# Optimization experiments

Measured on AMD Instinct MI355X. Metric: run time of the kernel, lower is better.

Reference implementation:

```python
import jax, jax.numpy as jnp
import numpy as np

INPUT_DIM = 24
HIDDEN = 128
NUM_LAYERS = 3
OUTPUT_DIM = 1


def _lstm_layer(x, Wih, Whh, bih, bhh):
    """Single LSTM layer, PyTorch gate order (i, f, g, o). x: [B,T,D] -> [B,T,H]."""
    B = x.shape[0]
    H = Whh.shape[1]
    # Precompute input projections for all timesteps at once: [B,T,4H]
    xg = jnp.einsum('btd,gd->btg', x, Wih) + bih
    xg = jnp.swapaxes(xg, 0, 1)  # [T,B,4H]
    h0 = jnp.zeros((B, H), x.dtype)
    c0 = jnp.zeros((B, H), x.dtype)

    def step(carry, xt):
        h, c = carry
        gates = xt + h @ Whh.T + bhh  # [B,4H]
        i, f, g, o = jnp.split(gates, 4, axis=-1)
        i = jax.nn.sigmoid(i)
        f = jax.nn.sigmoid(f)
        g = jnp.tanh(g)
        o = jax.nn.sigmoid(o)
        c = f * c + i * g
        h = o * jnp.tanh(c)
        return (h, c), h

    _, hs = jax.lax.scan(step, (h0, c0), xg)  # hs: [T,B,H]
    return jnp.swapaxes(hs, 0, 1)  # [B,T,H]


def setup_inputs() -> dict:
    key = jax.random.key(0)
    ks = jax.random.split(key, 16)
    B, T = 2048, 256
    s = 0.05
    inp = {
        'x': jax.random.normal(ks[0], (B, T, INPUT_DIM), dtype=jnp.float32),
    }
    dims_in = [INPUT_DIM, HIDDEN, HIDDEN]
    for l in range(NUM_LAYERS):
        inp[f'Wih{l}'] = jax.random.normal(ks[1 + 4 * l], (4 * HIDDEN, dims_in[l]), dtype=jnp.float32) * s
        inp[f'Whh{l}'] = jax.random.normal(ks[2 + 4 * l], (4 * HIDDEN, HIDDEN), dtype=jnp.float32) * s
        inp[f'bih{l}'] = jax.random.normal(ks[3 + 4 * l], (4 * HIDDEN,), dtype=jnp.float32) * s
        inp[f'bhh{l}'] = jax.random.normal(ks[4 + 4 * l], (4 * HIDDEN,), dtype=jnp.float32) * s
    inp['Wfc'] = jax.random.normal(ks[13], (OUTPUT_DIM, HIDDEN), dtype=jnp.float32) * s
    inp['bfc'] = jax.random.normal(ks[14], (OUTPUT_DIM,), dtype=jnp.float32) * s
    return inp


def reference(x, Wih0, Whh0, bih0, bhh0, Wih1, Whh1, bih1, bhh1,
              Wih2, Whh2, bih2, bhh2, Wfc, bfc):
    # 3 stacked LSTM layers (dropout inactive in eval mode), zero initial state.
    h = _lstm_layer(x, Wih0, Whh0, bih0, bhh0)
    h = _lstm_layer(h, Wih1, Whh1, bih1, bhh1)
    h = _lstm_layer(h, Wih2, Whh2, bih2, bhh2)
    # Linear projection of the final timestep: [B,1]
    return h[:, -1, :] @ Wfc.T + bfc
```

## Files before the change

### kernel.cpp

```cpp
#include <hip/hip_runtime.h>

#define T_STEPS 256
#define BATCH   2048
#define HID     128
#define ROWS    8

typedef short short8  __attribute__((ext_vector_type(8)));
typedef float float4v __attribute__((ext_vector_type(4)));

__device__ __forceinline__ unsigned short f2bf(float f) {
    unsigned int u = __builtin_bit_cast(unsigned int, f);
    u += 0x7fffu + ((u >> 16) & 1u);
    return (unsigned short)(u >> 16);
}
__device__ __forceinline__ float bf2f(unsigned short b) {
    unsigned int u = ((unsigned int)b) << 16;
    return __builtin_bit_cast(float, u);
}

#if __has_builtin(__builtin_amdgcn_exp2f)
#define EXP2F(x) __builtin_amdgcn_exp2f(x)
#else
#define EXP2F(x) exp2f(x)
#endif
__device__ __forceinline__ float sigf(float x) {
    return __builtin_amdgcn_rcpf(1.0f + EXP2F(x * -1.442695041f));
}
__device__ __forceinline__ float tanh_fast(float x) {
    return 2.0f * __builtin_amdgcn_rcpf(1.0f + EXP2F(x * -2.885390082f)) - 1.0f;
}

__device__ __forceinline__ void block_sync_lds() {
    asm volatile("s_waitcnt lgkmcnt(0)" ::: "memory");
    __builtin_amdgcn_s_barrier();
    __builtin_amdgcn_sched_barrier(0);
}

__device__ __forceinline__ int lpos(int row, int byteoff) {
    return (row * 512 + byteoff) ^ ((row & 7) << 4);
}

__device__ __forceinline__ short8 load_w8(const float* __restrict__ p) {
    float4v a = *reinterpret_cast<const float4v*>(p);
    float4v b = *reinterpret_cast<const float4v*>(p + 4);
    short8 r;
    r[0] = (short)f2bf(a[0]); r[1] = (short)f2bf(a[1]);
    r[2] = (short)f2bf(a[2]); r[3] = (short)f2bf(a[3]);
    r[4] = (short)f2bf(b[0]); r[5] = (short)f2bf(b[1]);
    r[6] = (short)f2bf(b[2]); r[7] = (short)f2bf(b[3]);
    return r;
}

template<bool IS_L0, bool WRITE_H, bool FINAL>
__global__ __launch_bounds__(512, 2)
void lstm_layer(const float* __restrict__ x0,
                const float* __restrict__ Wih,
                const float* __restrict__ Whh,
                const float* __restrict__ bih,
                const float* __restrict__ bhh,
                unsigned short* __restrict__ hbuf,
                const float* __restrict__ Wfc,
                const float* __restrict__ bfc,
                float* __restrict__ out)
{
    constexpr int KS_TOT = IS_L0 ? 5 : 8;
    constexpr int BUF = ROWS * 512;
    __shared__ __attribute__((aligned(16))) unsigned char a_lds[2 * BUF];

    const int tid   = threadIdx.x;
    const int lane  = tid & 63;
    const int wv    = tid >> 6;
    const int b0    = blockIdx.x * ROWS;

    const int t16   = lane & 15;
    const int kgrp8 = (lane >> 4) * 8;
    const int jcol  = 16 * wv + t16;
    const int m0    = (lane >> 4) * 4;
    const bool upper = (lane >= 32);
    const int rbase  = upper ? 2 : 0;
    const int row0   = (m0 & 7) + rbase;

    int aoff[KS_TOT];
    #pragma unroll
    for (int ks = 0; ks < KS_TOT; ++ks) {
        const int boff = (ks < 4) ? (ks * 64 + kgrp8 * 2)
                                  : (256 + (ks - 4) * 64 + kgrp8 * 2);
        aoff[ks] = lpos(t16 & 7, boff);
    }
    const int hwoff0 = lpos(row0,     2 * jcol);
    const int hwoff1 = lpos(row0 + 1, 2 * jcol);

    const int srow4 = tid >> 6, scol4 = tid & 63;
    const int hroff4 = lpos(srow4, scol4 * 4);
    const int sloff4 = lpos(srow4, 256 + scol4 * 4);
    const size_t sgoff4 = (size_t)(b0 + srow4) * HID + scol4 * 2;
    const int  xrow   = tid / 24, xe = tid % 24;
    const bool xvalid = tid < 192;
    const int  l0_loff = xvalid ? lpos(xrow, 256 + 2 * xe) : 0;
    const size_t l0_goff = xvalid ? ((size_t)(b0 + xrow) * (T_STEPS * 24) + xe) : 0;

    short8 wf[4][KS_TOT];
    float  bias[4];
    #pragma unroll
    for (int q = 0; q < 4; ++q) {
        const int n = 128 * q + jcol;
        bias[q] = bih[n] + bhh[n];
        #pragma unroll
        for (int ks = 0; ks < 4; ++ks)
            wf[q][ks] = load_w8(Whh + n * 128 + ks * 32 + kgrp8);
        if (IS_L0) {
            if (kgrp8 < 24) wf[q][4] = load_w8(Wih + n * 24 + kgrp8);
            else            { short8 z = {0,0,0,0,0,0,0,0}; wf[q][4] = z; }
        } else {
            #pragma unroll
            for (int ks = 4; ks < 8; ++ks)
                wf[q][ks] = load_w8(Wih + n * 128 + (ks - 4) * 32 + kgrp8);
        }
    }

    {
        short8 z = {0,0,0,0,0,0,0,0};
        *reinterpret_cast<short8*>(&a_lds[tid * 16]) = z;
    }
    __syncthreads();

    unsigned int xh = 0;
    float xf = 0.f;
    if (!IS_L0) {
        unsigned int v0 = *reinterpret_cast<const unsigned int*>(&hbuf[sgoff4]);
        *reinterpret_cast<unsigned int*>(&a_lds[sloff4]) = v0;
        xh = *reinterpret_cast<const unsigned int*>(&hbuf[(size_t)BATCH * HID + sgoff4]);
    } else if (xvalid) {
        float v0 = x0[l0_goff];
        *reinterpret_cast<unsigned short*>(&a_lds[l0_loff]) = f2bf(v0);
        xf = x0[l0_goff + 24];
    }
    __syncthreads();

    float creg[2] = {0.f, 0.f};

    auto step = [&](int t, int rb, int wb) {
        if (WRITE_H && t > 0) {
            unsigned int hv = *reinterpret_cast<const unsigned int*>(&a_lds[rb + hroff4]);
            *reinterpret_cast<unsigned int*>(
                &hbuf[(size_t)(t - 1) * (BATCH * HID) + sgoff4]) = hv;
        }
        if (t + 1 < T_STEPS) {
            if (!IS_L0)
                *reinterpret_cast<unsigned int*>(&a_lds[wb + sloff4]) = xh;
            else if (xvalid)
                *reinterpret_cast<unsigned short*>(&a_lds[wb + l0_loff]) = f2bf(xf);
        }
        if (t + 2 < T_STEPS) {
            if (!IS_L0)
                xh = *reinterpret_cast<const unsigned int*>(
                    &hbuf[(size_t)(t + 2) * (BATCH * HID) + sgoff4]);
            else if (xvalid)
                xf = x0[l0_goff + (size_t)(t + 2) * 24];
        }
        float4v acc[4];
        #pragma unroll
        for (int q = 0; q < 4; ++q)
            acc[q] = float4v{bias[q], bias[q], bias[q], bias[q]};
        __builtin_amdgcn_s_setprio(1);
        #pragma unroll
        for (int ks = 0; ks < KS_TOT; ++ks) {
            short8 av = *reinterpret_cast<const short8*>(&a_lds[rb + aoff[ks]]);
            #pragma unroll
            for (int q = 0; q < 4; ++q)
                acc[q] = __builtin_amdgcn_mfma_f32_16x16x32_bf16(av, wf[q][ks], acc[q], 0, 0, 0);
        }
        __builtin_amdgcn_s_setprio(0);
        float g0[4], g1[4];
        #pragma unroll
        for (int q = 0; q < 4; ++q) {
            g0[q] = upper ? acc[q][2] : acc[q][0];
            g1[q] = upper ? acc[q][3] : acc[q][1];
        }
        const float c0 = sigf(g0[1]) * creg[0] + sigf(g0[0]) * tanh_fast(g0[2]);
        const float c1 = sigf(g1[1]) * creg[1] + sigf(g1[0]) * tanh_fast(g1[2]);
        creg[0] = c0;  creg[1] = c1;
        const float h0 = sigf(g0[3]) * tanh_fast(c0);
        const float h1 = sigf(g1[3]) * tanh_fast(c1);
        unsigned int packed;
        asm("v_cvt_pk_bf16_f32 %0, %1, %2" : "=v"(packed) : "v"(h0), "v"(h1));
        *reinterpret_cast<unsigned short*>(&a_lds[wb + hwoff0]) =
            (unsigned short)(packed & 0xffffu);
        *reinterpret_cast<unsigned short*>(&a_lds[wb + hwoff1]) =
            (unsigned short)(packed >> 16);
        block_sync_lds();
    };

    for (int th = 0; th < T_STEPS / 2; ++th) {
        step(2 * th,     0,   BUF);
        step(2 * th + 1, BUF, 0);
    }
    if (WRITE_H) {
        unsigned int hv = *reinterpret_cast<const unsigned int*>(&a_lds[hroff4]);
        *reinterpret_cast<unsigned int*>(
            &hbuf[(size_t)(T_STEPS - 1) * (BATCH * HID) + sgoff4]) = hv;
    }
    if (FINAL && tid < 128) {
        const int r = tid >> 4, seg = tid & 15;
        float s = 0.f;
        #pragma unroll
        for (int k = 0; k < 8; ++k) {
            const int j = seg * 8 + k;
            s += bf2f(*reinterpret_cast<const unsigned short*>(&a_lds[lpos(r, 2 * j)]))
                 * Wfc[j];
        }
        #pragma unroll
        for (int off = 8; off >= 1; off >>= 1) s += __shfl_xor(s, off);
        if (seg == 0) out[b0 + r] = s + bfc[0];
    }
}

extern "C" void kernel_launch(void* const* d_in, const int* in_sizes, int n_in,
                              void* d_out, int out_size, void* d_ws, size_t ws_size,
                              hipStream_t stream) {
    (void)in_sizes; (void)n_in; (void)out_size; (void)ws_size;
    const float* x    = (const float*)d_in[0];
    const float* Wih0 = (const float*)d_in[1];
    const float* Whh0 = (const float*)d_in[2];
    const float* bih0 = (const float*)d_in[3];
    const float* bhh0 = (const float*)d_in[4];
    const float* Wih1 = (const float*)d_in[5];
    const float* Whh1 = (const float*)d_in[6];
    const float* bih1 = (const float*)d_in[7];
    const float* bhh1 = (const float*)d_in[8];
    const float* Wih2 = (const float*)d_in[9];
    const float* Whh2 = (const float*)d_in[10];
    const float* bih2 = (const float*)d_in[11];
    const float* bhh2 = (const float*)d_in[12];
    const float* Wfc  = (const float*)d_in[13];
    const float* bfc  = (const float*)d_in[14];
    float* out = (float*)d_out;
    unsigned short* hbuf = (unsigned short*)d_ws;

    dim3 grid(BATCH / ROWS), block(512);
    lstm_layer<true,  true,  false><<<grid, block, 0, stream>>>(x,       Wih0, Whh0, bih0, bhh0, hbuf, nullptr, nullptr, nullptr);
    lstm_layer<false, true,  false><<<grid, block, 0, stream>>>(nullptr, Wih1, Whh1, bih1, bhh1, hbuf, nullptr, nullptr, nullptr);
    lstm_layer<false, false, true ><<<grid, block, 0, stream>>>(nullptr, Wih2, Whh2, bih2, bhh2, hbuf, Wfc,     bfc,     out);
}
```

Baseline: 660.7 us.

## Feed input operand to MFMA directly from global registers, shrink LDS to h only

The input-side operand (the previous layer's h, or x for layer 0) is no longer staged through LDS. Each lane loads its MFMA A-fragment straight from global memory into registers, double-buffered one step ahead, and layer 0 converts x to bf16 in registers. The LDS buffer now holds only the recurrent h, halving LDS footprint and per-step LDS traffic. The trade-off is that each wave issues redundant global loads of the same input rows, which adds VGPR pressure and global bandwidth, and the prefetch distance drops from two steps to one.

Result: slower. 902.8 us (+36.6%).

```diff
diff --git a/kernel.cpp b/kernel.cpp
--- a/kernel.cpp
+++ b/kernel.cpp
@@ -7,6 +7,7 @@
 
 typedef short short8  __attribute__((ext_vector_type(8)));
 typedef float float4v __attribute__((ext_vector_type(4)));
+typedef unsigned int uint4v __attribute__((ext_vector_type(4)));
 
 __device__ __forceinline__ unsigned short f2bf(float f) {
     unsigned int u = __builtin_bit_cast(unsigned int, f);
@@ -36,8 +37,8 @@
     __builtin_amdgcn_sched_barrier(0);
 }
 
-__device__ __forceinline__ int lpos(int row, int byteoff) {
-    return (row * 512 + byteoff) ^ ((row & 7) << 4);
+__device__ __forceinline__ int lposR(int row, int byteoff) {
+    return (row * 256 + byteoff) ^ ((row & 7) << 4);
 }
 
 __device__ __forceinline__ short8 load_w8(const float* __restrict__ p) {
@@ -63,8 +64,8 @@
                 const float* __restrict__ bfc,
                 float* __restrict__ out)
 {
-    constexpr int KS_TOT = IS_L0 ? 5 : 8;
-    constexpr int BUF = ROWS * 512;
+    constexpr int KS_X  = IS_L0 ? 1 : 4;
+    constexpr int BUF   = ROWS * 256;
     __shared__ __attribute__((aligned(16))) unsigned char a_lds[2 * BUF];
 
     const int tid   = threadIdx.x;
@@ -75,31 +76,29 @@
     const int t16   = lane & 15;
     const int kgrp8 = (lane >> 4) * 8;
     const int jcol  = 16 * wv + t16;
-    const int m0    = (lane >> 4) * 4;
+    const int arow  = t16 & 7;
     const bool upper = (lane >= 32);
-    const int rbase  = upper ? 2 : 0;
-    const int row0   = (m0 & 7) + rbase;
-
-    int aoff[KS_TOT];
+    const int row0   = (((lane >> 4) * 4) & 7) + (upper ? 2 : 0);
+
+    int aoff[4];
     #pragma unroll
-    for (int ks = 0; ks < KS_TOT; ++ks) {
-        const int boff = (ks < 4) ? (ks * 64 + kgrp8 * 2)
-                                  : (256 + (ks - 4) * 64 + kgrp8 * 2);
-        aoff[ks] = lpos(t16 & 7, boff);
-    }
-    const int hwoff0 = lpos(row0,     2 * jcol);
-    const int hwoff1 = lpos(row0 + 1, 2 * jcol);
+    for (int ks = 0; ks < 4; ++ks)
+        aoff[ks] = lposR(arow, ks * 64 + kgrp8 * 2);
+    const int hwoff0 = lposR(row0,     2 * jcol);
+    const int hwoff1 = lposR(row0 + 1, 2 * jcol);
 
     const int srow4 = tid >> 6, scol4 = tid & 63;
-    const int hroff4 = lpos(srow4, scol4 * 4);
-    const int sloff4 = lpos(srow4, 256 + scol4 * 4);
+    const int hroff4 = lposR(srow4, scol4 * 4);
     const size_t sgoff4 = (size_t)(b0 + srow4) * HID + scol4 * 2;
-    const int  xrow   = tid / 24, xe = tid % 24;
-    const bool xvalid = tid < 192;
-    const int  l0_loff = xvalid ? lpos(xrow, 256 + 2 * xe) : 0;
-    const size_t l0_goff = xvalid ? ((size_t)(b0 + xrow) * (T_STEPS * 24) + xe) : 0;
-
-    short8 wf[4][KS_TOT];
+
+    size_t xgo[4];
+    #pragma unroll
+    for (int s = 0; s < 4; ++s)
+        xgo[s] = (size_t)(b0 + arow) * HID + s * 32 + kgrp8;
+    const bool xok = (kgrp8 < 24);
+    const size_t x0goff = (size_t)(b0 + arow) * (T_STEPS * 24) + (xok ? kgrp8 : 0);
+
+    short8 wf[4][4 + KS_X];
     float  bias[4];
     #pragma unroll
     for (int q = 0; q < 4; ++q) {
@@ -109,67 +108,87 @@
         for (int ks = 0; ks < 4; ++ks)
             wf[q][ks] = load_w8(Whh + n * 128 + ks * 32 + kgrp8);
         if (IS_L0) {
-            if (kgrp8 < 24) wf[q][4] = load_w8(Wih + n * 24 + kgrp8);
-            else            { short8 z = {0,0,0,0,0,0,0,0}; wf[q][4] = z; }
+            if (xok) wf[q][4] = load_w8(Wih + n * 24 + kgrp8);
+            else     { short8 z = {0,0,0,0,0,0,0,0}; wf[q][4] = z; }
         } else {
             #pragma unroll
-            for (int ks = 4; ks < 8; ++ks)
-                wf[q][ks] = load_w8(Wih + n * 128 + (ks - 4) * 32 + kgrp8);
+            for (int s = 0; s < 4; ++s)
+                wf[q][4 + s] = load_w8(Wih + n * 128 + s * 32 + kgrp8);
         }
     }
 
     {
-        short8 z = {0,0,0,0,0,0,0,0};
-        *reinterpret_cast<short8*>(&a_lds[tid * 16]) = z;
+        int2 z = {0, 0};
+        *reinterpret_cast<int2*>(&a_lds[tid * 8]) = z;
     }
     __syncthreads();
 
-    unsigned int xh = 0;
-    float xf = 0.f;
+    short8  xhA[4], xhB[4];
+    float4v xfA[2], xfB[2];
     if (!IS_L0) {
-        unsigned int v0 = *reinterpret_cast<const unsigned int*>(&hbuf[sgoff4]);
-        *reinterpret_cast<unsigned int*>(&a_lds[sloff4]) = v0;
-        xh = *reinterpret_cast<const unsigned int*>(&hbuf[(size_t)BATCH * HID + sgoff4]);
-    } else if (xvalid) {
-        float v0 = x0[l0_goff];
-        *reinterpret_cast<unsigned short*>(&a_lds[l0_loff]) = f2bf(v0);
-        xf = x0[l0_goff + 24];
-    }
-    __syncthreads();
+        #pragma unroll
+        for (int s = 0; s < 4; ++s)
+            xhA[s] = *reinterpret_cast<const short8*>(&hbuf[xgo[s]]);
+    } else {
+        const float* p = x0 + x0goff;
+        xfA[0] = *reinterpret_cast<const float4v*>(p);
+        xfA[1] = *reinterpret_cast<const float4v*>(p + 4);
+    }
 
     float creg[2] = {0.f, 0.f};
 
-    auto step = [&](int t, int rb, int wb) {
+    auto step = [&](int t, int rb, int wb,
+                    short8 (&xhc)[4], short8 (&xhn)[4],
+                    float4v (&xfc)[2], float4v (&xfn)[2]) {
         if (WRITE_H && t > 0) {
             unsigned int hv = *reinterpret_cast<const unsigned int*>(&a_lds[rb + hroff4]);
             *reinterpret_cast<unsigned int*>(
                 &hbuf[(size_t)(t - 1) * (BATCH * HID) + sgoff4]) = hv;
         }
         if (t + 1 < T_STEPS) {
-            if (!IS_L0)
-                *reinterpret_cast<unsigned int*>(&a_lds[wb + sloff4]) = xh;
-            else if (xvalid)
-                *reinterpret_cast<unsigned short*>(&a_lds[wb + l0_loff]) = f2bf(xf);
-        }
-        if (t + 2 < T_STEPS) {
-            if (!IS_L0)
-                xh = *reinterpret_cast<const unsigned int*>(
-                    &hbuf[(size_t)(t + 2) * (BATCH * HID) + sgoff4]);
-            else if (xvalid)
-                xf = x0[l0_goff + (size_t)(t + 2) * 24];
-        }
+            if constexpr (IS_L0) {
+                const float* p = x0 + x0goff + (size_t)(t + 1) * 24;
+                xfn[0] = *reinterpret_cast<const float4v*>(p);
+                xfn[1] = *reinterpret_cast<const float4v*>(p + 4);
+            } else {
+                #pragma unroll
+                for (int s = 0; s < 4; ++s)
+                    xhn[s] = *reinterpret_cast<const short8*>(
+                        &hbuf[(size_t)(t + 1) * (BATCH * HID) + xgo[s]]);
+            }
+        }
+        short8 hva[4];
+        #pragma unroll
+        for (int ks = 0; ks < 4; ++ks)
+            hva[ks] = *reinterpret_cast<const short8*>(&a_lds[rb + aoff[ks]]);
         float4v acc[4];
         #pragma unroll
         for (int q = 0; q < 4; ++q)
             acc[q] = float4v{bias[q], bias[q], bias[q], bias[q]};
         __builtin_amdgcn_s_setprio(1);
-        #pragma unroll
-        for (int ks = 0; ks < KS_TOT; ++ks) {
-            short8 av = *reinterpret_cast<const short8*>(&a_lds[rb + aoff[ks]]);
+        if constexpr (IS_L0) {
+            unsigned int u0, u1, u2, u3;
+            asm("v_cvt_pk_bf16_f32 %0, %1, %2" : "=v"(u0) : "v"(xfc[0][0]), "v"(xfc[0][1]));
+            asm("v_cvt_pk_bf16_f32 %0, %1, %2" : "=v"(u1) : "v"(xfc[0][2]), "v"(xfc[0][3]));
+            asm("v_cvt_pk_bf16_f32 %0, %1, %2" : "=v"(u2) : "v"(xfc[1][0]), "v"(xfc[1][1]));
+            asm("v_cvt_pk_bf16_f32 %0, %1, %2" : "=v"(u3) : "v"(xfc[1][2]), "v"(xfc[1][3]));
+            uint4v xu = {u0, u1, u2, u3};
+            short8 av = __builtin_bit_cast(short8, xu);
             #pragma unroll
             for (int q = 0; q < 4; ++q)
-                acc[q] = __builtin_amdgcn_mfma_f32_16x16x32_bf16(av, wf[q][ks], acc[q], 0, 0, 0);
-        }
+                acc[q] = __builtin_amdgcn_mfma_f32_16x16x32_bf16(av, wf[q][4], acc[q], 0, 0, 0);
+        } else {
+            #pragma unroll
+            for (int s = 0; s < 4; ++s)
+                #pragma unroll
+                for (int q = 0; q < 4; ++q)
+                    acc[q] = __builtin_amdgcn_mfma_f32_16x16x32_bf16(xhc[s], wf[q][4 + s], acc[q], 0, 0, 0);
+        }
+        #pragma unroll
+        for (int ks = 0; ks < 4; ++ks)
+            #pragma unroll
+            for (int q = 0; q < 4; ++q)
+                acc[q] = __builtin_amdgcn_mfma_f32_16x16x32_bf16(hva[ks], wf[q][ks], acc[q], 0, 0, 0);
         __builtin_amdgcn_s_setprio(0);
         float g0[4], g1[4];
         #pragma unroll
@@ -192,8 +211,8 @@
     };
 
     for (int th = 0; th < T_STEPS / 2; ++th) {
-        step(2 * th,     0,   BUF);
-        step(2 * th + 1, BUF, 0);
+        step(2 * th,     0,   BUF, xhA, xhB, xfA, xfB);
+        step(2 * th + 1, BUF, 0,   xhB, xhA, xfB, xfA);
     }
     if (WRITE_H) {
         unsigned int hv = *reinterpret_cast<const unsigned int*>(&a_lds[hroff4]);
@@ -206,7 +225,7 @@
         #pragma unroll
         for (int k = 0; k < 8; ++k) {
             const int j = seg * 8 + k;
-            s += bf2f(*reinterpret_cast<const unsigned short*>(&a_lds[lpos(r, 2 * j)]))
+            s += bf2f(*reinterpret_cast<const unsigned short*>(&a_lds[lposR(r, 2 * j)]))
                  * Wfc[j];
         }
         #pragma unroll
```
